# Optimization experiments

Hardware: AMD Instinct MI355X
Metric: run time of the kernel (lower is better)

## Reference

```python
import jax, jax.numpy as jnp
import numpy as np

DEGREE = 5
LN_EPS = 1e-5


def _xavier(key, shape):
    fan_in, fan_out = shape[-1] if len(shape) == 2 else shape[1] * shape[2], shape[0]
    limit = float(np.sqrt(6.0 / (fan_in + fan_out)))
    return jax.random.uniform(key, shape, jnp.float32, -limit, limit)


def setup_inputs() -> dict:
    key = jax.random.key(0)
    ks = jax.random.split(key, 6)
    B, D0, D1, D2 = 16384, 1024, 1024, 512
    return {
        "x": jax.random.normal(ks[0], (B, D0), jnp.float32),
        "coeff1": _xavier(ks[1], (D1, D0, DEGREE + 1)),
        "base_w1": _xavier(ks[2], (D1, D0)),
        "bias1": jnp.zeros((D1,), jnp.float32),
        "ln_gamma": jnp.ones((D1,), jnp.float32),
        "ln_beta": jnp.zeros((D1,), jnp.float32),
        "coeff2": _xavier(ks[3], (D2, D1, DEGREE + 1)),
        "base_w2": _xavier(ks[4], (D2, D1)),
        "bias2": jnp.zeros((D2,), jnp.float32),
    }


def _cheb_layer(x, coeff, base_w, bias):
    # x: [B, I]; coeff: [O, I, D+1]; base_w: [O, I]; bias: [O]
    xn = jnp.tanh(x)
    polys = [jnp.ones_like(xn), xn]
    for _ in range(2, DEGREE + 1):
        polys.append(2.0 * xn * polys[-1] - polys[-2])
    cheb = jnp.stack(polys, axis=-1)  # [B, I, D+1]
    y = jnp.einsum("bid,oid->bo", cheb, coeff)
    y = y + x @ base_w.T + bias
    return y


def _layernorm(h, gamma, beta):
    mu = jnp.mean(h, axis=-1, keepdims=True)
    var = jnp.mean(jnp.square(h - mu), axis=-1, keepdims=True)
    return (h - mu) * jax.lax.rsqrt(var + LN_EPS) * gamma + beta


def reference(x, coeff1, base_w1, bias1, ln_gamma, ln_beta, coeff2, base_w2, bias2):
    x = jnp.tanh(x)  # input_normalization='tanh'
    h = _cheb_layer(x, coeff1, base_w1, bias1)
    h = _layernorm(h, ln_gamma, ln_beta)
    h = h * jax.nn.sigmoid(h)  # SiLU
    out = _cheb_layer(h, coeff2, base_w2, bias2)
    return out
```

## Files before the change

kernel.cpp:

```cpp
#include <hip/hip_runtime.h>


typedef __bf16 bf16x8 __attribute__((ext_vector_type(8)));
typedef float f32x4 __attribute__((ext_vector_type(4)));
typedef unsigned short u16x8 __attribute__((ext_vector_type(8)));

__device__ __forceinline__ unsigned short f2bf(float f) {
    unsigned int u = __float_as_uint(f);
    unsigned int r = (u + 0x7FFFu + ((u >> 16) & 1u)) >> 16;
    return (unsigned short)r;
}
__device__ __forceinline__ float bf2f(unsigned short b) {
    return __uint_as_float(((unsigned int)b) << 16);
}

__device__ __forceinline__ float fast_tanh(float x) {
    float a = fminf(fmaxf(x, -15.f), 15.f);
    float e = __expf(2.f * a);
    return 1.f - 2.f * __builtin_amdgcn_rcpf(e + 1.f);
}
__device__ __forceinline__ float fast_silu(float y) {
    float a = fminf(fmaxf(y, -30.f), 30.f);
    return y * __builtin_amdgcn_rcpf(1.f + __expf(-a));
}

__device__ __forceinline__ void cheb_pack(float s, unsigned short* o6) {
    float u  = fast_tanh(s);
    float T1 = u;
    float T2 = 2.f * u * u - 1.f;
    float T3 = 2.f * u * T2 - T1;
    float T4 = 2.f * u * T3 - T2;
    float T5 = 2.f * u * T4 - T3;
    o6[0] = f2bf(T1); o6[1] = f2bf(T2); o6[2] = f2bf(T3);
    o6[3] = f2bf(T4); o6[4] = f2bf(T5); o6[5] = f2bf(s);
}

__device__ __forceinline__ void load_lds16(const void* g, void* l) {
    __builtin_amdgcn_global_load_lds(
        (const __attribute__((address_space(1))) void*)g,
        (__attribute__((address_space(3))) void*)l, 16, 0, 0);
}

__global__ __launch_bounds__(256) void prep_w_kernel(
    const float* __restrict__ coeff, const float* __restrict__ base_w,
    unsigned short* __restrict__ W, int OI)
{
    int idx = blockIdx.x * 256 + threadIdx.x;
    if (idx >= OI) return;
    const float* c = coeff + (size_t)idx * 6;
    unsigned short w0 = f2bf(c[1]), w1 = f2bf(c[2]), w2 = f2bf(c[3]),
                   w3 = f2bf(c[4]), w4 = f2bf(c[5]), w5 = f2bf(base_w[idx]);
    unsigned int* d = (unsigned int*)(W + (size_t)idx * 6);
    d[0] = w0 | ((unsigned int)w1 << 16);
    d[1] = w2 | ((unsigned int)w3 << 16);
    d[2] = w4 | ((unsigned int)w5 << 16);
}

__global__ __launch_bounds__(256) void prep_bias_kernel(
    const float* __restrict__ coeff, const float* __restrict__ bias,
    float* __restrict__ bp, int I)
{
    int o = blockIdx.x, tid = threadIdx.x;
    float s = 0.f;
    for (int i = tid; i < I; i += 256) s += coeff[((size_t)o * I + i) * 6];
    #pragma unroll
    for (int off = 32; off > 0; off >>= 1) s += __shfl_down(s, off);
    __shared__ float red[4];
    int lane = tid & 63, wv = tid >> 6;
    if (lane == 0) red[wv] = s;
    __syncthreads();
    if (tid == 0) bp[o] = bias[o] + red[0] + red[1] + red[2] + red[3];
}

__global__ __launch_bounds__(256) void expand1_kernel(
    const float* __restrict__ x, unsigned short* __restrict__ Xa)
{
    int b = blockIdx.x, tid = threadIdx.x;
    f32x4 xv = *(const f32x4*)(x + (size_t)b * 1024 + tid * 4);
    alignas(16) unsigned short ov[24];
    #pragma unroll
    for (int e = 0; e < 4; e++) cheb_pack(fast_tanh(xv[e]), ov + e * 6);
    u16x8* dst = (u16x8*)(Xa + (size_t)b * 6144 + tid * 24);
    const u16x8* src = (const u16x8*)ov;
    dst[0] = src[0]; dst[1] = src[1]; dst[2] = src[2];
}

__global__ __launch_bounds__(256) void ln_silu_expand_kernel(
    const unsigned short* __restrict__ H, const float* __restrict__ gamma,
    const float* __restrict__ beta, unsigned short* __restrict__ Xa)
{
    int b = blockIdx.x, tid = threadIdx.x;
    ushort4 hb = *(const ushort4*)(H + (size_t)b * 1024 + tid * 4);
    float hv[4] = { bf2f(hb.x), bf2f(hb.y), bf2f(hb.z), bf2f(hb.w) };
    float s1 = hv[0] + hv[1] + hv[2] + hv[3];
    float s2 = hv[0]*hv[0] + hv[1]*hv[1] + hv[2]*hv[2] + hv[3]*hv[3];
    #pragma unroll
    for (int off = 32; off > 0; off >>= 1) {
        s1 += __shfl_down(s1, off);
        s2 += __shfl_down(s2, off);
    }
    __shared__ float red[8];
    __shared__ float stats[2];
    int lane = tid & 63, wv = tid >> 6;
    if (lane == 0) { red[wv] = s1; red[4 + wv] = s2; }
    __syncthreads();
    if (tid == 0) {
        float t1 = red[0] + red[1] + red[2] + red[3];
        float t2 = red[4] + red[5] + red[6] + red[7];
        float mu = t1 * (1.f / 1024.f);
        float var = t2 * (1.f / 1024.f) - mu * mu;
        stats[0] = mu;
        stats[1] = rsqrtf(var + 1e-5f);
    }
    __syncthreads();
    float mu = stats[0], rs = stats[1];
    f32x4 g  = *(const f32x4*)(gamma + tid * 4);
    f32x4 bt = *(const f32x4*)(beta  + tid * 4);
    alignas(16) unsigned short ov[24];
    #pragma unroll
    for (int e = 0; e < 4; e++) {
        float y = (hv[e] - mu) * rs * g[e] + bt[e];
        cheb_pack(fast_silu(y), ov + e * 6);
    }
    u16x8* dst = (u16x8*)(Xa + (size_t)b * 6144 + tid * 24);
    const u16x8* src = (const u16x8*)ov;
    dst[0] = src[0]; dst[1] = src[1]; dst[2] = src[2];
}


#define WAITTOP() do { \
    asm volatile("s_waitcnt vmcnt(0) lgkmcnt(0)" ::: "memory"); \
    __builtin_amdgcn_s_barrier(); } while (0)

template<int BN, bool OUT_BF16>
__global__ __launch_bounds__(512, 2) void gemm3_kernel(
    const unsigned short* __restrict__ A,
    const unsigned short* __restrict__ Wt,
    const float* __restrict__ bias,
    void* __restrict__ Cout,
    int N, int K, int NMT)
{
    constexpr int FN  = BN / 64;
    constexpr int ASZ = 256 * 32;
    constexpr int BSZ = BN * 32;
    __shared__ __align__(16) unsigned short As[2 * ASZ];
    __shared__ __align__(16) unsigned short Bs[2 * BSZ];

    const int tid  = threadIdx.x;
    const int lane = tid & 63;
    const int wave = tid >> 6;
    const int wm   = wave >> 2;
    const int wn   = wave & 3;

    int wg = blockIdx.x;
    {
        const int nwg = gridDim.x;
        if ((nwg & 7) == 0) { const int cpx = nwg >> 3; wg = (wg & 7) * cpx + (wg >> 3); }
    }
    const int mt = wg % NMT;
    const int nt = wg / NMT;
    const size_t m0 = (size_t)mt * 256;
    const size_t n0 = (size_t)nt * BN;

    const int cs   = (((lane & 3) ^ ((lane >> 3) & 3)) << 3);
    const int srow = lane >> 2;
    const unsigned short* AgJ0 = A + (m0 + (size_t)((wave * 2 + 0) * 16 + srow)) * K + cs;
    const unsigned short* AgJ1 = A + (m0 + (size_t)((wave * 2 + 1) * 16 + srow)) * K + cs;
    const unsigned short* BgJ0 = Wt + (n0 + (size_t)((wave * (BN / 128) + 0) * 16 + srow)) * K + cs;
    const unsigned short* BgJ1 = (BN == 256)
        ? Wt + (n0 + (size_t)((wave * 2 + 1) * 16 + srow)) * K + cs : BgJ0;
    unsigned short* AD0 = As + (wave * 2 + 0) * 512 + lane * 8;
    unsigned short* AD1 = As + (wave * 2 + 1) * 512 + lane * 8;
    unsigned short* BD0 = Bs + (wave * (BN / 128) + 0) * 512 + lane * 8;
    unsigned short* BD1 = Bs + (wave * 2 + 1) * 512 + lane * 8;

    const int fr = lane & 15;
    const int cg = lane >> 4;
    const int ck = ((cg ^ ((fr >> 1) & 3)) << 3);
    const unsigned short* PA = As + (wm * 128 + fr) * 32 + ck;
    const unsigned short* PB = Bs + (wn * (BN / 4) + fr) * 32 + ck;

    const int NT = K >> 5;

    f32x4 acc[2][4][FN];
    #pragma unroll
    for (int mh = 0; mh < 2; ++mh)
        #pragma unroll
        for (int mf = 0; mf < 4; ++mf)
            #pragma unroll
            for (int nf = 0; nf < FN; ++nf)
                acc[mh][mf][nf] = f32x4{0.f, 0.f, 0.f, 0.f};

    bf16x8 aF[8], aG[8], bF[FN], bG[FN];

#define STAGE(T, B_) do { \
    const size_t ko_ = (size_t)(T) * 32; \
    load_lds16(AgJ0 + ko_, AD0 + (B_) * ASZ); \
    load_lds16(AgJ1 + ko_, AD1 + (B_) * ASZ); \
    load_lds16(BgJ0 + ko_, BD0 + (B_) * BSZ); \
    if constexpr (BN == 256) load_lds16(BgJ1 + ko_, BD1 + (B_) * BSZ); \
} while (0)

#define RD(AF_, BF_, B_) do { \
    _Pragma("unroll") \
    for (int mh = 0; mh < 2; ++mh) \
        _Pragma("unroll") \
        for (int mf = 0; mf < 4; ++mf) \
            AF_[mh * 4 + mf] = *(const bf16x8*)(PA + (B_) * ASZ + (mh * 64 + mf * 16) * 32); \
    _Pragma("unroll") \
    for (int nf = 0; nf < FN; ++nf) \
        BF_[nf] = *(const bf16x8*)(PB + (B_) * BSZ + nf * 16 * 32); \
} while (0)

#define MM(AF_, BF_) do { \
    _Pragma("unroll") \
    for (int mh = 0; mh < 2; ++mh) \
        _Pragma("unroll") \
        for (int mf = 0; mf < 4; ++mf) \
            _Pragma("unroll") \
            for (int nf = 0; nf < FN; ++nf) \
                acc[mh][mf][nf] = __builtin_amdgcn_mfma_f32_16x16x32_bf16( \
                    AF_[mh * 4 + mf], BF_[nf], acc[mh][mf][nf], 0, 0, 0); \
} while (0)

    STAGE(0, 0);
    STAGE(1, 1);
    if constexpr (BN == 256) asm volatile("s_waitcnt vmcnt(4)" ::: "memory");
    else                     asm volatile("s_waitcnt vmcnt(3)" ::: "memory");
    __builtin_amdgcn_s_barrier();
    RD(aF, bF, 0);

    for (int t = 0; t < NT - 2; t += 2) {
        WAITTOP();
        RD(aG, bG, 1);
        STAGE(t + 2, 0);
        MM(aF, bF);
        WAITTOP();
        RD(aF, bF, 0);
        STAGE(t + 3, 1);
        MM(aG, bG);
    }
    WAITTOP();
    RD(aG, bG, 1);
    MM(aF, bF);
    WAITTOP();
    MM(aG, bG);

#undef STAGE
#undef RD
#undef MM

    const size_t rbase0 = m0 + wm * 128 + ((lane >> 4) << 2);
    const int cb = lane & 15;
    int colg[FN]; float bv[FN];
    #pragma unroll
    for (int nf = 0; nf < FN; ++nf) {
        colg[nf] = (int)n0 + wn * (BN / 4) + nf * 16 + cb;
        bv[nf] = bias[colg[nf]];
    }
    #pragma unroll
    for (int mh = 0; mh < 2; ++mh)
        #pragma unroll
        for (int mf = 0; mf < 4; ++mf) {
            const size_t rg0 = rbase0 + mh * 64 + mf * 16;
            #pragma unroll
            for (int r = 0; r < 4; ++r) {
                const size_t rowoff = (rg0 + r) * (size_t)N;
                #pragma unroll
                for (int nf = 0; nf < FN; ++nf) {
                    const float v = acc[mh][mf][nf][r] + bv[nf];
                    if constexpr (OUT_BF16)
                        ((unsigned short*)Cout)[rowoff + colg[nf]] = f2bf(v);
                    else
                        ((float*)Cout)[rowoff + colg[nf]] = v;
                }
            }
        }
}

extern "C" void kernel_launch(void* const* d_in, const int* in_sizes, int n_in,
                              void* d_out, int out_size, void* d_ws, size_t ws_size,
                              hipStream_t stream)
{
    const float* x       = (const float*)d_in[0];
    const float* coeff1  = (const float*)d_in[1];
    const float* base_w1 = (const float*)d_in[2];
    const float* bias1   = (const float*)d_in[3];
    const float* gamma   = (const float*)d_in[4];
    const float* beta    = (const float*)d_in[5];
    const float* coeff2  = (const float*)d_in[6];
    const float* base_w2 = (const float*)d_in[7];
    const float* bias2   = (const float*)d_in[8];
    float* out = (float*)d_out;

    const int B = 16384, D0 = 1024, D1 = 1024, D2 = 512;
    const int K1 = D0 * 6, K2 = D1 * 6;

    char* base = (char*)d_ws;
    size_t off = 0;
    unsigned short* W1 = (unsigned short*)(base + off); off += (size_t)D1 * K1 * 2;
    unsigned short* W2 = (unsigned short*)(base + off); off += (size_t)D2 * K2 * 2;
    float* b1p = (float*)(base + off); off += (size_t)D1 * 4;
    float* b2p = (float*)(base + off); off += (size_t)D2 * 4;
    off = (off + 255) & ~(size_t)255;

    size_t per_row = (size_t)K1 * 2 + (size_t)D1 * 2;
    long long avail = (long long)ws_size - (long long)off;
    long long mcl = avail > 0 ? avail / (long long)per_row : 0;
    int Mc = (int)((mcl / 256) * 256);
    if (Mc < 256) Mc = 256;
    if (Mc > B) Mc = B;

    unsigned short* Xa = (unsigned short*)(base + off);
    unsigned short* h = (unsigned short*)(base + off + (size_t)Mc * K1 * 2);

    prep_w_kernel<<<(D1 * D0 + 255) / 256, 256, 0, stream>>>(coeff1, base_w1, W1, D1 * D0);
    prep_w_kernel<<<(D2 * D1 + 255) / 256, 256, 0, stream>>>(coeff2, base_w2, W2, D2 * D1);
    prep_bias_kernel<<<D1, 256, 0, stream>>>(coeff1, bias1, b1p, D0);
    prep_bias_kernel<<<D2, 256, 0, stream>>>(coeff2, bias2, b2p, D1);

    for (int m0 = 0; m0 < B; m0 += Mc) {
        int rows = (B - m0 < Mc) ? (B - m0) : Mc;
        int nmt = rows / 256;
        expand1_kernel<<<rows, 256, 0, stream>>>(x + (size_t)m0 * D0, Xa);
        gemm3_kernel<256, true><<<nmt * (D1 / 256), 512, 0, stream>>>(
            Xa, W1, b1p, h, D1, K1, nmt);
        ln_silu_expand_kernel<<<rows, 256, 0, stream>>>(h, gamma, beta, Xa);
        gemm3_kernel<128, false><<<nmt * (D2 / 128), 512, 0, stream>>>(
            Xa, W2, b2p, out + (size_t)m0 * D2, D2, K2, nmt);
    }
}
```

Before: 714.8 us.

## Deepen GEMM LDS pipeline from double to quad buffering with partial waits

The GEMM kernel now keeps four K-stages in shared memory instead of two. Its barriers wait only until the next stage's global-to-LDS loads have landed (partial vmcnt), rather than draining every outstanding load. The goal is to hide global memory latency by keeping more loads in flight across MFMA work. The cost is double the LDS footprint, which likely leaves room for only one 512-thread workgroup per CU instead of the two the launch bounds ask for, reducing occupancy.

```diff
diff --git a/kernel.cpp b/kernel.cpp
--- a/kernel.cpp
+++ b/kernel.cpp
@@ -128,12 +128,8 @@
 }
 
 
-#define WAITTOP() do { \
-    asm volatile("s_waitcnt vmcnt(0) lgkmcnt(0)" ::: "memory"); \
-    __builtin_amdgcn_s_barrier(); } while (0)
-
 template<int BN, bool OUT_BF16>
-__global__ __launch_bounds__(512, 2) void gemm3_kernel(
+__global__ __launch_bounds__(512, 2) void gemm4_kernel(
     const unsigned short* __restrict__ A,
     const unsigned short* __restrict__ Wt,
     const float* __restrict__ bias,
@@ -141,10 +137,11 @@
     int N, int K, int NMT)
 {
     constexpr int FN  = BN / 64;
+    constexpr int LPS = 2 + BN / 128;
     constexpr int ASZ = 256 * 32;
     constexpr int BSZ = BN * 32;
-    __shared__ __align__(16) unsigned short As[2 * ASZ];
-    __shared__ __align__(16) unsigned short Bs[2 * BSZ];
+    __shared__ __align__(16) unsigned short As[4 * ASZ];
+    __shared__ __align__(16) unsigned short Bs[4 * BSZ];
 
     const int tid  = threadIdx.x;
     const int lane = tid & 63;
@@ -193,23 +190,23 @@
 
     bf16x8 aF[8], aG[8], bF[FN], bG[FN];
 
-#define STAGE(T, B_) do { \
+#define STAGE(T, R_) do { \
     const size_t ko_ = (size_t)(T) * 32; \
-    load_lds16(AgJ0 + ko_, AD0 + (B_) * ASZ); \
-    load_lds16(AgJ1 + ko_, AD1 + (B_) * ASZ); \
-    load_lds16(BgJ0 + ko_, BD0 + (B_) * BSZ); \
-    if constexpr (BN == 256) load_lds16(BgJ1 + ko_, BD1 + (B_) * BSZ); \
+    load_lds16(AgJ0 + ko_, AD0 + (R_) * ASZ); \
+    load_lds16(AgJ1 + ko_, AD1 + (R_) * ASZ); \
+    load_lds16(BgJ0 + ko_, BD0 + (R_) * BSZ); \
+    if constexpr (BN == 256) load_lds16(BgJ1 + ko_, BD1 + (R_) * BSZ); \
 } while (0)
 
-#define RD(AF_, BF_, B_) do { \
+#define RD(AF_, BF_, R_) do { \
     _Pragma("unroll") \
     for (int mh = 0; mh < 2; ++mh) \
         _Pragma("unroll") \
         for (int mf = 0; mf < 4; ++mf) \
-            AF_[mh * 4 + mf] = *(const bf16x8*)(PA + (B_) * ASZ + (mh * 64 + mf * 16) * 32); \
+            AF_[mh * 4 + mf] = *(const bf16x8*)(PA + (R_) * ASZ + (mh * 64 + mf * 16) * 32); \
     _Pragma("unroll") \
     for (int nf = 0; nf < FN; ++nf) \
-        BF_[nf] = *(const bf16x8*)(PB + (B_) * BSZ + nf * 16 * 32); \
+        BF_[nf] = *(const bf16x8*)(PB + (R_) * BSZ + nf * 16 * 32); \
 } while (0)
 
 #define MM(AF_, BF_) do { \
@@ -223,32 +220,41 @@
                     AF_[mh * 4 + mf], BF_[nf], acc[mh][mf][nf], 0, 0, 0); \
 } while (0)
 
-    STAGE(0, 0);
-    STAGE(1, 1);
-    if constexpr (BN == 256) asm volatile("s_waitcnt vmcnt(4)" ::: "memory");
-    else                     asm volatile("s_waitcnt vmcnt(3)" ::: "memory");
+#define WSTEADY() do { \
+    if constexpr (BN == 256) asm volatile("s_waitcnt vmcnt(8) lgkmcnt(0)" ::: "memory"); \
+    else                     asm volatile("s_waitcnt vmcnt(6) lgkmcnt(0)" ::: "memory"); \
+    __builtin_amdgcn_s_barrier(); } while (0)
+#define WTAIL1() do { \
+    if constexpr (BN == 256) asm volatile("s_waitcnt vmcnt(4) lgkmcnt(0)" ::: "memory"); \
+    else                     asm volatile("s_waitcnt vmcnt(3) lgkmcnt(0)" ::: "memory"); \
+    __builtin_amdgcn_s_barrier(); } while (0)
+#define WTAIL0() do { \
+    asm volatile("s_waitcnt vmcnt(0) lgkmcnt(0)" ::: "memory"); \
+    __builtin_amdgcn_s_barrier(); } while (0)
+
+    STAGE(0, 0); STAGE(1, 1); STAGE(2, 2); STAGE(3, 3);
+    if constexpr (BN == 256) asm volatile("s_waitcnt vmcnt(12)" ::: "memory");
+    else                     asm volatile("s_waitcnt vmcnt(9)" ::: "memory");
     __builtin_amdgcn_s_barrier();
     RD(aF, bF, 0);
 
-    for (int t = 0; t < NT - 2; t += 2) {
-        WAITTOP();
-        RD(aG, bG, 1);
-        STAGE(t + 2, 0);
-        MM(aF, bF);
-        WAITTOP();
-        RD(aF, bF, 0);
-        STAGE(t + 3, 1);
-        MM(aG, bG);
-    }
-    WAITTOP();
-    RD(aG, bG, 1);
-    MM(aF, bF);
-    WAITTOP();
+    for (int t = 0; t < NT - 4; t += 4) {
+        WSTEADY(); RD(aG, bG, 1); STAGE(t + 4, 0); MM(aF, bF);
+        WSTEADY(); RD(aF, bF, 2); STAGE(t + 5, 1); MM(aG, bG);
+        WSTEADY(); RD(aG, bG, 3); STAGE(t + 6, 2); MM(aF, bF);
+        WSTEADY(); RD(aF, bF, 0); STAGE(t + 7, 3); MM(aG, bG);
+    }
+    WSTEADY(); RD(aG, bG, 1); MM(aF, bF);
+    WTAIL1();  RD(aF, bF, 2); MM(aG, bG);
+    WTAIL0();  RD(aG, bG, 3); MM(aF, bF);
     MM(aG, bG);
 
 #undef STAGE
 #undef RD
 #undef MM
+#undef WSTEADY
+#undef WTAIL1
+#undef WTAIL0
 
     const size_t rbase0 = m0 + wm * 128 + ((lane >> 4) << 2);
     const int cb = lane & 15;
@@ -323,10 +329,10 @@
         int rows = (B - m0 < Mc) ? (B - m0) : Mc;
         int nmt = rows / 256;
         expand1_kernel<<<rows, 256, 0, stream>>>(x + (size_t)m0 * D0, Xa);
-        gemm3_kernel<256, true><<<nmt * (D1 / 256), 512, 0, stream>>>(
+        gemm4_kernel<256, true><<<nmt * (D1 / 256), 512, 0, stream>>>(
             Xa, W1, b1p, h, D1, K1, nmt);
         ln_silu_expand_kernel<<<rows, 256, 0, stream>>>(h, gamma, beta, Xa);
-        gemm3_kernel<128, false><<<nmt * (D2 / 128), 512, 0, stream>>>(
+        gemm4_kernel<128, false><<<nmt * (D2 / 128), 512, 0, stream>>>(
             Xa, W2, b2p, out + (size_t)m0 * D2, D2, K2, nmt);
     }
 }
```

Result: faster. 650.1 us (-9.1%).
